# Performance work log

Hardware: AMD Instinct MI355X
Metric: run time of the kernel (lower is better)

The kernel has to match this reference:

```python
import jax, jax.numpy as jnp
import numpy as np

DIFF_Q = 0.8
ONE_OVER_DIFF_TOT = 0.05234482976098482
N_LAYER = 4


def setup_inputs() -> dict:
    key = jax.random.key(0)
    ks = jax.random.split(key, 6)
    B, N = 8, 32768
    x = jax.random.normal(ks[0], (B, N, 26, 4), dtype=jnp.float32)
    # torch Linear convention: W has shape [out, in], y = x @ W.T + b
    Ws = jax.random.normal(ks[1], (N_LAYER, 16, 16), dtype=jnp.float32) * 0.25
    bs = jax.random.normal(ks[2], (N_LAYER, 16), dtype=jnp.float32) * 0.1
    Wf = jax.random.normal(ks[3], (1, 16), dtype=jnp.float32) * 0.25
    bf = jax.random.normal(ks[4], (1,), dtype=jnp.float32) * 0.1
    extra = jax.random.uniform(ks[5], (12,), dtype=jnp.float32)
    return {"x": x, "Ws": Ws, "bs": bs, "Wf": Wf, "bf": bf, "extra": extra}


def _net(h, Ws, bs, Wf, bf):
    for i in range(N_LAYER):
        h = jnp.tanh(jnp.einsum('bnci,oi->bnco', h, Ws[i]) + bs[i])
    return jnp.einsum('bnci,oi->bnco', h, Wf) + bf  # [B,N,26,1]


def reference(x, Ws, bs, Wf, bf, extra):
    B, N = x.shape[0], x.shape[1]
    b = jnp.broadcast_to(extra, (B, N, 26, 12))
    x1 = jnp.concatenate([x, b], axis=3)                                   # [B,N,26,16]
    x2 = jnp.concatenate([x[..., 2:], x[..., :2], b], axis=3)              # [B,N,26,16]
    y = jnp.tanh(_net(x1, Ws, bs, Wf, bf) - _net(x2, Ws, bs, Wf, bf))      # [B,N,26,1]
    y = jnp.squeeze(y, axis=3)
    t = jnp.sum(y, axis=2) * (ONE_OVER_DIFF_TOT * DIFF_Q)                  # [B,N]
    return t
```

## Files before the change

kernel.cpp:

```cpp
#include <hip/hip_runtime.h>

typedef __fp16   fp16x2  __attribute__((ext_vector_type(2)));
typedef _Float16 half4   __attribute__((ext_vector_type(4)));
typedef float    floatx4 __attribute__((ext_vector_type(4)));

__device__ __forceinline__ float act_pre(float a) {
    float r = __builtin_amdgcn_rcpf(__builtin_amdgcn_exp2f(a) + 1.0f);
    return fmaf(-2.0f, r, 1.0f);
}

__device__ __forceinline__ floatx4 ract4(floatx4 a) {
    float d0 = __builtin_amdgcn_exp2f(a[0]) + 1.0f;
    float d1 = __builtin_amdgcn_exp2f(a[1]) + 1.0f;
    float d2 = __builtin_amdgcn_exp2f(a[2]) + 1.0f;
    float d3 = __builtin_amdgcn_exp2f(a[3]) + 1.0f;
    float p1 = d0 * d1;
    float p2 = p1 * d2;
    float p3 = p2 * d3;
    float q3 = __builtin_amdgcn_rcpf(p3);
    float r3 = q3 * p2;
    float q2 = q3 * d3;
    float r2 = q2 * p1;
    float q1 = q2 * d2;
    float r1 = q1 * d0;
    float r0 = q1 * d1;
    floatx4 r = {r0, r1, r2, r3};
    return r;
}

__device__ __forceinline__ half4 mk4f(floatx4 v) {
    fp16x2 lo = __builtin_amdgcn_cvt_pkrtz(v[0], v[1]);
    fp16x2 hi = __builtin_amdgcn_cvt_pkrtz(v[2], v[3]);
    union { fp16x2 h2[2]; half4 h4; } u;
    u.h2[0] = lo; u.h2[1] = hi;
    return u.h4;
}

__global__ __launch_bounds__(256, 4) void automaton_kernel(
    const float* __restrict__ x, const float* __restrict__ Ws,
    const float* __restrict__ bs, const float* __restrict__ Wf,
    const float* __restrict__ bf, const float* __restrict__ extra,
    float* __restrict__ out, int n_groups)
{
    const float K = 2.885390081777927f;
    const int tid   = blockIdx.x * blockDim.x + threadIdx.x;
    const int wave  = tid >> 6;
    const int lane  = threadIdx.x & 63;
    const int col   = lane & 15;
    const int sub   = lane >> 4;
    const int obase = sub * 4;

    const floatx4 zeroC = {0.f, 0.f, 0.f, 0.f};
    const half4   ones  = {(_Float16)1.f, (_Float16)1.f, (_Float16)1.f, (_Float16)1.f};

    float ex[12];
#pragma unroll
    for (int j = 0; j < 12; ++j) ex[j] = extra[j];

    float W0c[4][4], c1[4];
#pragma unroll
    for (int e = 0; e < 4; ++e) {
        const float* row = Ws + (obase + e) * 16;
        floatx4 r0 = *(const floatx4*)(row);
        floatx4 r1 = *(const floatx4*)(row + 4);
        floatx4 r2 = *(const floatx4*)(row + 8);
        floatx4 r3 = *(const floatx4*)(row + 12);
#pragma unroll
        for (int j = 0; j < 4; ++j) W0c[e][j] = r0[j] * K;
        float c = bs[obase + e];
#pragma unroll
        for (int j = 0; j < 4; ++j) c = fmaf(r1[j], ex[j], c);
#pragma unroll
        for (int j = 0; j < 4; ++j) c = fmaf(r2[j], ex[4 + j], c);
#pragma unroll
        for (int j = 0; j < 4; ++j) c = fmaf(r3[j], ex[8 + j], c);
        c1[e] = c * K;
    }

    half4 aW0, aW1, aW2, aWf;
    floatx4 bC0, bC1, bC2;
    {
        floatx4 w1 = *(const floatx4*)(Ws + 256 + col * 16 + obase);
        floatx4 w2 = *(const floatx4*)(Ws + 512 + col * 16 + obase);
        floatx4 w3 = *(const floatx4*)(Ws + 768 + col * 16 + obase);
#pragma unroll
        for (int e = 0; e < 4; ++e) {
            aW0[e] = (_Float16)(w1[e] * (-2.0f * K));
            aW1[e] = (_Float16)(w2[e] * (-2.0f * K));
            aW2[e] = (_Float16)(w3[e] * (-2.0f * K));
        }
        floatx4 s0 = __builtin_amdgcn_mfma_f32_16x16x16f16(aW0, ones, zeroC, 0, 0, 0);
        floatx4 s1 = __builtin_amdgcn_mfma_f32_16x16x16f16(aW1, ones, zeroC, 0, 0, 0);
        floatx4 s2 = __builtin_amdgcn_mfma_f32_16x16x16f16(aW2, ones, zeroC, 0, 0, 0);
        floatx4 b1 = *(const floatx4*)(bs + 16 + obase);
        floatx4 b2 = *(const floatx4*)(bs + 32 + obase);
        floatx4 b3 = *(const floatx4*)(bs + 48 + obase);
#pragma unroll
        for (int e = 0; e < 4; ++e) {
            bC0[e] = fmaf(-0.5f, s0[e], K * b1[e]);
            bC1[e] = fmaf(-0.5f, s1[e], K * b2[e]);
            bC2[e] = fmaf(-0.5f, s2[e], K * b3[e]);
        }
        floatx4 wf = *(const floatx4*)(Wf + obase);
#pragma unroll
        for (int e = 0; e < 4; ++e) aWf[e] = (_Float16)(wf[e] * (-2.0f * K));
    }

    const int g      = wave * 16 + col;
    const bool valid = (g < n_groups);
    const int gl     = valid ? g : (n_groups - 1);
    const float* xp  = x + (size_t)gl * 104;

    float acc = 0.0f;
#pragma unroll
    for (int c = 0; c < 26; ++c) {
        floatx4 xv = *(const floatx4*)(xp + c * 4);

        floatx4 z1, z2;
#pragma unroll
        for (int e = 0; e < 4; ++e) {
            float a1 = c1[e];
            a1 = fmaf(W0c[e][0], xv[0], a1);
            a1 = fmaf(W0c[e][1], xv[1], a1);
            a1 = fmaf(W0c[e][2], xv[2], a1);
            a1 = fmaf(W0c[e][3], xv[3], a1);
            float a2 = c1[e];
            a2 = fmaf(W0c[e][0], xv[2], a2);
            a2 = fmaf(W0c[e][1], xv[3], a2);
            a2 = fmaf(W0c[e][2], xv[0], a2);
            a2 = fmaf(W0c[e][3], xv[1], a2);
            z1[e] = a1; z2[e] = a2;
        }
        half4 hb1 = mk4f(ract4(z1));
        half4 hb2 = mk4f(ract4(z2));

        {
            floatx4 d1 = __builtin_amdgcn_mfma_f32_16x16x16f16(aW0, hb1, bC0, 0, 0, 0);
            floatx4 d2 = __builtin_amdgcn_mfma_f32_16x16x16f16(aW0, hb2, bC0, 0, 0, 0);
            hb1 = mk4f(ract4(d1));
            hb2 = mk4f(ract4(d2));
        }
        {
            floatx4 d1 = __builtin_amdgcn_mfma_f32_16x16x16f16(aW1, hb1, bC1, 0, 0, 0);
            floatx4 d2 = __builtin_amdgcn_mfma_f32_16x16x16f16(aW1, hb2, bC1, 0, 0, 0);
            hb1 = mk4f(ract4(d1));
            hb2 = mk4f(ract4(d2));
        }

        {
            floatx4 d1 = __builtin_amdgcn_mfma_f32_16x16x16f16(aW2, hb1, bC2, 0, 0, 0);
            floatx4 d2 = __builtin_amdgcn_mfma_f32_16x16x16f16(aW2, hb2, bC2, 0, 0, 0);
            floatx4 rv1 = ract4(d1);
            floatx4 rv2 = ract4(d2);
            floatx4 s = rv1 - rv2;
            half4 sb = mk4f(s);
            floatx4 dr = __builtin_amdgcn_mfma_f32_16x16x16f16(aWf, sb, zeroC, 0, 0, 0);
            acc += act_pre(dr[0]);
        }
    }
    if (lane < 16 && valid)
        out[g] = acc * 0.041875863808787856f;
}

extern "C" void kernel_launch(void* const* d_in, const int* in_sizes, int n_in,
                              void* d_out, int out_size, void* d_ws, size_t ws_size,
                              hipStream_t stream) {
    const float* x  = (const float*)d_in[0];
    const float* Ws = (const float*)d_in[1];
    const float* bs = (const float*)d_in[2];
    const float* Wf = (const float*)d_in[3];
    const float* bf = (const float*)d_in[4];
    const float* ex = (const float*)d_in[5];
    float* out = (float*)d_out;

    const int n_groups = out_size;
    const int waves    = (n_groups + 15) / 16;
    const int blocks   = (waves + 3) / 4;
    automaton_kernel<<<blocks, 256, 0, stream>>>(x, Ws, bs, Wf, bf, ex, out, n_groups);
}
```

Measured before the change: 171.8 us.

## Pair sigmoid reciprocals across branches and software-prefetch x in partially unrolled loop

New measurement: 166.4 us. 3.1% less time.

```diff
diff --git a/kernel.cpp b/kernel.cpp
--- a/kernel.cpp
+++ b/kernel.cpp
@@ -2,6 +2,7 @@
 
 typedef __fp16   fp16x2  __attribute__((ext_vector_type(2)));
 typedef _Float16 half4   __attribute__((ext_vector_type(4)));
+typedef float    floatx2 __attribute__((ext_vector_type(2)));
 typedef float    floatx4 __attribute__((ext_vector_type(4)));
 
 __device__ __forceinline__ float act_pre(float a) {
@@ -9,22 +10,11 @@
     return fmaf(-2.0f, r, 1.0f);
 }
 
-__device__ __forceinline__ floatx4 ract4(floatx4 a) {
-    float d0 = __builtin_amdgcn_exp2f(a[0]) + 1.0f;
-    float d1 = __builtin_amdgcn_exp2f(a[1]) + 1.0f;
-    float d2 = __builtin_amdgcn_exp2f(a[2]) + 1.0f;
-    float d3 = __builtin_amdgcn_exp2f(a[3]) + 1.0f;
-    float p1 = d0 * d1;
-    float p2 = p1 * d2;
-    float p3 = p2 * d3;
-    float q3 = __builtin_amdgcn_rcpf(p3);
-    float r3 = q3 * p2;
-    float q2 = q3 * d3;
-    float r2 = q2 * p1;
-    float q1 = q2 * d2;
-    float r1 = q1 * d0;
-    float r0 = q1 * d1;
-    floatx4 r = {r0, r1, r2, r3};
+__device__ __forceinline__ floatx2 ract2(float a1, float a2) {
+    float d1 = __builtin_amdgcn_exp2f(a1) + 1.0f;
+    float d2 = __builtin_amdgcn_exp2f(a2) + 1.0f;
+    float q  = __builtin_amdgcn_rcpf(d1 * d2);
+    floatx2 r = {q * d2, q * d1};
     return r;
 }
 
@@ -112,51 +102,74 @@
     const float* xp  = x + (size_t)gl * 104;
 
     float acc = 0.0f;
+    floatx4 xv = *(const floatx4*)(xp);
+#pragma unroll 2
+    for (int c = 0; c < 26; ++c) {
+        floatx4 xn = (c < 25) ? *(const floatx4*)(xp + (c + 1) * 4) : xv;
+
+        floatx4 rv1, rv2;
+        {
+            floatx4 z1, z2;
 #pragma unroll
-    for (int c = 0; c < 26; ++c) {
-        floatx4 xv = *(const floatx4*)(xp + c * 4);
-
-        floatx4 z1, z2;
+            for (int e = 0; e < 4; ++e) {
+                float a1 = c1[e];
+                a1 = fmaf(W0c[e][0], xv[0], a1);
+                a1 = fmaf(W0c[e][1], xv[1], a1);
+                a1 = fmaf(W0c[e][2], xv[2], a1);
+                a1 = fmaf(W0c[e][3], xv[3], a1);
+                float a2 = c1[e];
+                a2 = fmaf(W0c[e][0], xv[2], a2);
+                a2 = fmaf(W0c[e][1], xv[3], a2);
+                a2 = fmaf(W0c[e][2], xv[0], a2);
+                a2 = fmaf(W0c[e][3], xv[1], a2);
+                z1[e] = a1; z2[e] = a2;
+            }
 #pragma unroll
-        for (int e = 0; e < 4; ++e) {
-            float a1 = c1[e];
-            a1 = fmaf(W0c[e][0], xv[0], a1);
-            a1 = fmaf(W0c[e][1], xv[1], a1);
-            a1 = fmaf(W0c[e][2], xv[2], a1);
-            a1 = fmaf(W0c[e][3], xv[3], a1);
-            float a2 = c1[e];
-            a2 = fmaf(W0c[e][0], xv[2], a2);
-            a2 = fmaf(W0c[e][1], xv[3], a2);
-            a2 = fmaf(W0c[e][2], xv[0], a2);
-            a2 = fmaf(W0c[e][3], xv[1], a2);
-            z1[e] = a1; z2[e] = a2;
+            for (int e = 0; e < 4; ++e) {
+                floatx2 rr = ract2(z1[e], z2[e]);
+                rv1[e] = rr[0]; rv2[e] = rr[1];
+            }
         }
-        half4 hb1 = mk4f(ract4(z1));
-        half4 hb2 = mk4f(ract4(z2));
+        half4 hb1 = mk4f(rv1);
+        half4 hb2 = mk4f(rv2);
 
         {
             floatx4 d1 = __builtin_amdgcn_mfma_f32_16x16x16f16(aW0, hb1, bC0, 0, 0, 0);
             floatx4 d2 = __builtin_amdgcn_mfma_f32_16x16x16f16(aW0, hb2, bC0, 0, 0, 0);
-            hb1 = mk4f(ract4(d1));
-            hb2 = mk4f(ract4(d2));
+#pragma unroll
+            for (int e = 0; e < 4; ++e) {
+                floatx2 rr = ract2(d1[e], d2[e]);
+                rv1[e] = rr[0]; rv2[e] = rr[1];
+            }
+            hb1 = mk4f(rv1);
+            hb2 = mk4f(rv2);
         }
         {
             floatx4 d1 = __builtin_amdgcn_mfma_f32_16x16x16f16(aW1, hb1, bC1, 0, 0, 0);
             floatx4 d2 = __builtin_amdgcn_mfma_f32_16x16x16f16(aW1, hb2, bC1, 0, 0, 0);
-            hb1 = mk4f(ract4(d1));
-            hb2 = mk4f(ract4(d2));
+#pragma unroll
+            for (int e = 0; e < 4; ++e) {
+                floatx2 rr = ract2(d1[e], d2[e]);
+                rv1[e] = rr[0]; rv2[e] = rr[1];
+            }
+            hb1 = mk4f(rv1);
+            hb2 = mk4f(rv2);
         }
 
         {
             floatx4 d1 = __builtin_amdgcn_mfma_f32_16x16x16f16(aW2, hb1, bC2, 0, 0, 0);
             floatx4 d2 = __builtin_amdgcn_mfma_f32_16x16x16f16(aW2, hb2, bC2, 0, 0, 0);
-            floatx4 rv1 = ract4(d1);
-            floatx4 rv2 = ract4(d2);
+#pragma unroll
+            for (int e = 0; e < 4; ++e) {
+                floatx2 rr = ract2(d1[e], d2[e]);
+                rv1[e] = rr[0]; rv2[e] = rr[1];
+            }
             floatx4 s = rv1 - rv2;
             half4 sb = mk4f(s);
             floatx4 dr = __builtin_amdgcn_mfma_f32_16x16x16f16(aWf, sb, zeroC, 0, 0, 0);
             acc += act_pre(dr[0]);
         }
+        xv = xn;
     }
     if (lane < 16 && valid)
         out[g] = acc * 0.041875863808787856f;
```
